# Optimization experiments

Measured on AMD Instinct MI355X. Metric: run time of the kernel, lower is better.

## Reference

```python
import jax, jax.numpy as jnp
import numpy as np

B, H, S, D = 2, 16, 2048, 128


def setup_inputs() -> dict:
    key = jax.random.key(0)
    kq, kk, kv = jax.random.split(key, 3)
    q = jax.random.normal(kq, (B, H, S, D), dtype=jnp.float32)
    k = jax.random.normal(kk, (B, H, S, D), dtype=jnp.float32)
    v = jax.random.normal(kv, (B, H, S, D), dtype=jnp.float32)
    scale = jnp.float32(1.0 / np.sqrt(D))
    return {"q": q, "k": k, "v": v, "scale": scale}


def reference(q, k, v, scale):
    # scores: [B, H, S, S]
    attn = jnp.einsum("bhqd,bhkd->bhqk", q, k) * scale
    attn = jnp.square(jax.nn.relu(attn))  # relu(x)^2 score function (no softmax)
    return jnp.einsum("bhqk,bhkd->bhqd", attn, v)
```

## Files before the change

### kernel.cpp

```cpp
#include <hip/hip_runtime.h>
#include <hip/hip_bf16.h>
#include <stdint.h>

#define S_LEN 2048
#define D_DIM 128
#define QT 128
#define KT 64
#define NT (S_LEN/KT)

typedef float  f32x4  __attribute__((ext_vector_type(4)));
typedef float  f32x16 __attribute__((ext_vector_type(16)));
typedef short  bf16x8 __attribute__((ext_vector_type(8)));
typedef unsigned int uintx4 __attribute__((ext_vector_type(4)));

__device__ __forceinline__ short f2bf(float f) {
    return __builtin_bit_cast(short, __float2bfloat16(f));
}

__device__ __forceinline__ unsigned int pk2(float lo, float hi) {
    unsigned int d;
    asm("v_cvt_pk_bf16_f32 %0, %1, %2" : "=v"(d) : "v"(lo), "v"(hi));
    return d;
}

__device__ __forceinline__ void gload_lds16(const short* g, char* l) {
    __builtin_amdgcn_global_load_lds(
        (const __attribute__((address_space(1))) void*)g,
        (__attribute__((address_space(3))) void*)l,
        16, 0, 0);
}

__global__ __launch_bounds__(256)
void convert_k_kernel(const float* __restrict__ kin, short* __restrict__ kbf) {
    const size_t i = ((size_t)blockIdx.x * 256 + threadIdx.x) * 8;
    f32x4 a = *(const f32x4*)(kin + i);
    f32x4 c = *(const f32x4*)(kin + i + 4);
    bf16x8 t;
    t[0]=f2bf(a[0]); t[1]=f2bf(a[1]); t[2]=f2bf(a[2]); t[3]=f2bf(a[3]);
    t[4]=f2bf(c[0]); t[5]=f2bf(c[1]); t[6]=f2bf(c[2]); t[7]=f2bf(c[3]);
    *(bf16x8*)(kbf + i) = t;
}

__global__ __launch_bounds__(256)
void transpose_v_kernel(const float* __restrict__ vin, short* __restrict__ vt) {
    __shared__ short T[16 * 130];
    const int tid = threadIdx.x;
    const int blk = blockIdx.x;
    const int bh  = blk >> 3;
    const int d0  = (blk & 7) * 16;
    const float* vb = vin + (size_t)bh * S_LEN * D_DIM;
    short* vtb = vt + (size_t)bh * (size_t)D_DIM * S_LEN;
    const int c4 = tid & 3;
    const int rr = tid >> 2;
    const int dl = tid >> 4;
    const int kc = tid & 15;

    for (int kc0 = 0; kc0 < S_LEN; kc0 += 128) {
        #pragma unroll
        for (int h = 0; h < 2; ++h) {
            const int krow = kc0 + h*64 + rr;
            f32x4 a = *(const f32x4*)(vb + (size_t)krow * D_DIM + d0 + c4*4);
            #pragma unroll
            for (int j = 0; j < 4; ++j)
                T[(c4*4 + j)*130 + h*64 + rr] = f2bf(a[j]);
        }
        __syncthreads();
        int w0 = *(const int*)&T[dl*130 + kc*8 + 0];
        int w1 = *(const int*)&T[dl*130 + kc*8 + 2];
        int w2 = *(const int*)&T[dl*130 + kc*8 + 4];
        int w3 = *(const int*)&T[dl*130 + kc*8 + 6];
        int4 val = make_int4(w0, w1, w2, w3);
        *(int4*)(vtb + (size_t)(d0 + dl) * S_LEN + kc0 + kc*8) = val;
        __syncthreads();
    }
}

__global__ __launch_bounds__(256, 2)
void relu2_attn_main(const float* __restrict__ q,
                     const short* __restrict__ kbf,
                     const short* __restrict__ vtbf,
                     const float* __restrict__ scale_p,
                     float* __restrict__ out) {
    __shared__ __align__(16) char lds[65536];

    const int tid  = threadIdx.x;
    const int wave = tid >> 6;
    const int lane = tid & 63;
    const int l31  = lane & 31;
    const int hi   = lane >> 5;

    const int bid = blockIdx.x;
    const int bh  = bid & 31;
    const int qt  = bid >> 5;
    const int q0  = qt * QT;

    const float* qb = q    + (size_t)bh * S_LEN * D_DIM;
    const short* kb = kbf  + (size_t)bh * S_LEN * D_DIM;
    const short* vt = vtbf + (size_t)bh * (size_t)D_DIM * S_LEN;
    float*       ob = out  + (size_t)bh * S_LEN * D_DIM;

    const float scale = scale_p[0];

    const int RB = hi*512 + l31*16;

    int kOff[4], vOff[4];
    #pragma unroll
    for (int p = 0; p < 4; ++p) {
        const int s = (p*4 + wave)*64 + lane;
        const int rK = ((s >> 9) << 5) | (s & 31);
        const int cK = (s >> 5) & 15;
        kOff[p] = rK*128 + cK*8;
        const int dV = (((s >> 8) & 3) << 5) | (s & 31);
        const int cV = (s >> 5) & 7;
        vOff[p] = dV*2048 + cV*8;
    }

    bf16x8 qa[8];
    {
        const int qrow = q0 + wave*32 + l31;
        const float* qp = qb + (size_t)qrow * D_DIM + hi*8;
        #pragma unroll
        for (int dk = 0; dk < 8; ++dk) {
            f32x4 a = *(const f32x4*)(qp + dk*16);
            f32x4 c = *(const f32x4*)(qp + dk*16 + 4);
            bf16x8 t;
            t[0]=f2bf(a[0]*scale); t[1]=f2bf(a[1]*scale);
            t[2]=f2bf(a[2]*scale); t[3]=f2bf(a[3]*scale);
            t[4]=f2bf(c[0]*scale); t[5]=f2bf(c[1]*scale);
            t[6]=f2bf(c[2]*scale); t[7]=f2bf(c[3]*scale);
            qa[dk] = t;
        }
    }

    f32x16 oacc[4];
    #pragma unroll
    for (int df = 0; df < 4; ++df) oacc[df] = {};

#define STAGE(T, B) do {                                                      \
    const int k0_ = (T) * KT;                                                 \
    _Pragma("unroll")                                                         \
    for (int p_ = 0; p_ < 4; ++p_) {                                          \
        const int ch_ = p_*4 + wave;                                          \
        gload_lds16(kb + k0_*128 + kOff[p_],                                  \
                    lds + (B)*16384 + ch_*1024);                              \
        gload_lds16(vt + k0_ + vOff[p_],                                      \
                    lds + 32768 + (B)*16384 + ch_*1024);                      \
    }                                                                         \
} while (0)

#define TILE_COMPUTE(BUF) do {                                                \
    f32x16 s0 = {}, s1 = {};                                                  \
    __builtin_amdgcn_s_setprio(1);                                            \
    _Pragma("unroll")                                                         \
    for (int dk = 0; dk < 8; ++dk) {                                          \
        bf16x8 a0 = *(const bf16x8*)(lds + (BUF)*16384 + RB + (dk<<10));      \
        bf16x8 a1 = *(const bf16x8*)(lds + (BUF)*16384 + RB + (dk<<10) + 8192); \
        s0 = __builtin_amdgcn_mfma_f32_32x32x16_bf16(a0, qa[dk], s0, 0, 0, 0);\
        s1 = __builtin_amdgcn_mfma_f32_32x32x16_bf16(a1, qa[dk], s1, 0, 0, 0);\
    }                                                                         \
    __builtin_amdgcn_s_setprio(0);                                            \
              \
    bf16x8 pa[4];                                                             \
    _Pragma("unroll")                                                         \
    for (int kf = 0; kf < 2; ++kf) {                                          \
        const f32x16 sv = kf ? s1 : s0;                                       \
        float pr[16];                                                         \
        _Pragma("unroll")                                                     \
        for (int r = 0; r < 16; ++r) {                                        \
            float m_ = fmaxf(sv[r], 0.f); pr[r] = m_ * m_;                    \
        }                                                                     \
        _Pragma("unroll")                                                     \
        for (int t2 = 0; t2 < 2; ++t2) {                                      \
            unsigned int X  = pk2(pr[8*t2+0], pr[8*t2+1]);                    \
            unsigned int Y  = pk2(pr[8*t2+4], pr[8*t2+5]);                    \
            unsigned int X2 = pk2(pr[8*t2+2], pr[8*t2+3]);                    \
            unsigned int Y2 = pk2(pr[8*t2+6], pr[8*t2+7]);                    \
            asm volatile("v_permlane32_swap_b32 %0, %1" : "+v"(X),  "+v"(Y)); \
            asm volatile("v_permlane32_swap_b32 %0, %1" : "+v"(X2), "+v"(Y2));\
            pa[kf*2 + t2] = __builtin_bit_cast(bf16x8, (uintx4){X, X2, Y, Y2});\
        }                                                                     \
    }                                                                         \
    __builtin_amdgcn_s_setprio(1);                                            \
    _Pragma("unroll")                                                         \
    for (int s_ = 0; s_ < 4; ++s_) {                                          \
        _Pragma("unroll")                                                     \
        for (int df = 0; df < 4; ++df) {                                      \
            bf16x8 vf = *(const bf16x8*)(lds + 32768 + (BUF)*16384 + RB       \
                                         + (df<<12) + (s_<<10));              \
            oacc[df] = __builtin_amdgcn_mfma_f32_32x32x16_bf16(pa[s_], vf, oacc[df], 0, 0, 0); \
        }                                                                     \
    }                                                                         \
    __builtin_amdgcn_s_setprio(0);                                            \
} while (0)

    STAGE(0, 0);

    #pragma unroll 1
    for (int p = 0; p < NT/2; ++p) {
        __syncthreads();
        STAGE(2*p + 1, 1);
        TILE_COMPUTE(0);
        __syncthreads();
        STAGE((2*p + 2) & (NT - 1), 0);
        TILE_COMPUTE(1);
    }

    #pragma unroll
    for (int df = 0; df < 4; ++df) {
        #pragma unroll
        for (int rg = 0; rg < 4; ++rg) {
            #pragma unroll
            for (int e = 0; e < 4; ++e) {
                const int row = q0 + wave*32 + rg*8 + hi*4 + e;
                ob[(size_t)row * D_DIM + df*32 + l31] = oacc[df][rg*4 + e];
            }
        }
    }
}

#define KS 136
#define VS 72
#define PS 72

__global__ __launch_bounds__(256, 2)
void relu2_attn_fallback(const float* __restrict__ q,
                         const float* __restrict__ k,
                         const float* __restrict__ v,
                         const float* __restrict__ scale_p,
                         float* __restrict__ out) {
    __shared__ short Klds[KT][KS];
    __shared__ short VTlds[D_DIM][VS];
    __shared__ short Plds[QT][PS];

    const int tid  = threadIdx.x;
    const int wave = tid >> 6;
    const int lane = tid & 63;
    const int l15  = lane & 15;
    const int lg   = lane >> 4;

    const int bid = blockIdx.x;
    const int bh  = bid & 31;
    const int qt  = bid >> 5;
    const int q0  = qt * QT;

    const float* qb = q + (size_t)bh * S_LEN * D_DIM;
    const float* kb = k + (size_t)bh * S_LEN * D_DIM;
    const float* vb = v + (size_t)bh * S_LEN * D_DIM;
    float*       ob = out + (size_t)bh * S_LEN * D_DIM;

    const float scale = scale_p[0];

    bf16x8 qa[2][4];
    {
        const int qrow = q0 + wave * 32;
        #pragma unroll
        for (int qf = 0; qf < 2; ++qf) {
            const float* qp = qb + (size_t)(qrow + qf*16 + l15) * D_DIM + lg * 8;
            #pragma unroll
            for (int dk = 0; dk < 4; ++dk) {
                f32x4 a = *(const f32x4*)(qp + dk*32);
                f32x4 c = *(const f32x4*)(qp + dk*32 + 4);
                bf16x8 t;
                t[0]=f2bf(a[0]*scale); t[1]=f2bf(a[1]*scale);
                t[2]=f2bf(a[2]*scale); t[3]=f2bf(a[3]*scale);
                t[4]=f2bf(c[0]*scale); t[5]=f2bf(c[1]*scale);
                t[6]=f2bf(c[2]*scale); t[7]=f2bf(c[3]*scale);
                qa[qf][dk] = t;
            }
        }
    }

    const int kr = tid >> 4;
    const int kc = tid & 15;
    const int vd = tid & 127;
    const int vh = (tid >> 7) * 32;

    f32x4 kreg[8];
    float vreg[32];

#define FLOAD_TILE(T) do {                                                    \
    const float* kp_ = kb + (size_t)((T) * KT) * D_DIM;                       \
    _Pragma("unroll")                                                         \
    for (int p = 0; p < 4; ++p) {                                             \
        const float* rp_ = kp_ + (size_t)(p*16 + kr) * D_DIM + kc*8;          \
        kreg[2*p]   = *(const f32x4*)rp_;                                     \
        kreg[2*p+1] = *(const f32x4*)(rp_ + 4);                               \
    }                                                                         \
    const float* vp_ = vb + (size_t)((T) * KT + vh) * D_DIM + vd;             \
    _Pragma("unroll")                                                         \
    for (int j = 0; j < 32; ++j) vreg[j] = vp_[(size_t)j * D_DIM];            \
} while (0)

#define FSTORE_TILE() do {                                                    \
    _Pragma("unroll")                                                         \
    for (int p = 0; p < 4; ++p) {                                             \
        f32x4 a_ = kreg[2*p], b_ = kreg[2*p+1];                               \
        bf16x8 w_;                                                            \
        w_[0]=f2bf(a_[0]); w_[1]=f2bf(a_[1]); w_[2]=f2bf(a_[2]); w_[3]=f2bf(a_[3]); \
        w_[4]=f2bf(b_[0]); w_[5]=f2bf(b_[1]); w_[6]=f2bf(b_[2]); w_[7]=f2bf(b_[3]); \
        *(bf16x8*)&Klds[p*16 + kr][kc*8] = w_;                                \
    }                                                                         \
    _Pragma("unroll")                                                         \
    for (int c = 0; c < 4; ++c) {                                             \
        bf16x8 w_;                                                            \
        w_[0]=f2bf(vreg[c*8+0]); w_[1]=f2bf(vreg[c*8+1]);                     \
        w_[2]=f2bf(vreg[c*8+2]); w_[3]=f2bf(vreg[c*8+3]);                     \
        w_[4]=f2bf(vreg[c*8+4]); w_[5]=f2bf(vreg[c*8+5]);                     \
        w_[6]=f2bf(vreg[c*8+6]); w_[7]=f2bf(vreg[c*8+7]);                     \
        *(bf16x8*)&VTlds[vd][vh + c*8] = w_;                                  \
    }                                                                         \
} while (0)

    f32x4 oacc[2][8];
    #pragma unroll
    for (int i = 0; i < 2; ++i)
        #pragma unroll
        for (int j = 0; j < 8; ++j)
            oacc[i][j] = f32x4{0.f, 0.f, 0.f, 0.f};

    FLOAD_TILE(0);

    for (int t = 0; t < NT; ++t) {
        FSTORE_TILE();
        __syncthreads();
        FLOAD_TILE((t + 1) & (NT - 1));

        f32x4 sacc[2][4];
        #pragma unroll
        for (int qf = 0; qf < 2; ++qf)
            #pragma unroll
            for (int kf = 0; kf < 4; ++kf)
                sacc[qf][kf] = f32x4{0.f, 0.f, 0.f, 0.f};

        #pragma unroll
        for (int dk = 0; dk < 4; ++dk) {
            #pragma unroll
            for (int kf = 0; kf < 4; ++kf) {
                bf16x8 bf = *(const bf16x8*)&Klds[kf*16 + l15][dk*32 + lg*8];
                #pragma unroll
                for (int qf = 0; qf < 2; ++qf)
                    sacc[qf][kf] = __builtin_amdgcn_mfma_f32_16x16x32_bf16(
                        qa[qf][dk], bf, sacc[qf][kf], 0, 0, 0);
            }
        }

        #pragma unroll
        for (int qf = 0; qf < 2; ++qf) {
            #pragma unroll
            for (int kf = 0; kf < 4; ++kf) {
                f32x4 sv = sacc[qf][kf];
                #pragma unroll
                for (int e = 0; e < 4; ++e) {
                    float r = fmaxf(sv[e], 0.f);
                    Plds[wave*32 + qf*16 + lg*4 + e][kf*16 + l15] = f2bf(r * r);
                }
            }
        }

        #pragma unroll
        for (int ks = 0; ks < 2; ++ks) {
            bf16x8 pa[2];
            #pragma unroll
            for (int qf = 0; qf < 2; ++qf)
                pa[qf] = *(const bf16x8*)&Plds[wave*32 + qf*16 + l15][ks*32 + lg*8];
            #pragma unroll
            for (int df = 0; df < 8; ++df) {
                bf16x8 vf = *(const bf16x8*)&VTlds[df*16 + l15][ks*32 + lg*8];
                #pragma unroll
                for (int qf = 0; qf < 2; ++qf)
                    oacc[qf][df] = __builtin_amdgcn_mfma_f32_16x16x32_bf16(
                        pa[qf], vf, oacc[qf][df], 0, 0, 0);
            }
        }
        __syncthreads();
    }

    #pragma unroll
    for (int qf = 0; qf < 2; ++qf) {
        #pragma unroll
        for (int df = 0; df < 8; ++df) {
            f32x4 o = oacc[qf][df];
            const int row = q0 + wave*32 + qf*16 + lg*4;
            float* op = ob + (size_t)row * D_DIM + df*16 + l15;
            op[0*D_DIM] = o[0];
            op[1*D_DIM] = o[1];
            op[2*D_DIM] = o[2];
            op[3*D_DIM] = o[3];
        }
    }
}

extern "C" void kernel_launch(void* const* d_in, const int* in_sizes, int n_in,
                              void* d_out, int out_size, void* d_ws, size_t ws_size,
                              hipStream_t stream) {
    const float* q = (const float*)d_in[0];
    const float* k = (const float*)d_in[1];
    const float* v = (const float*)d_in[2];
    const float* scale = (const float*)d_in[3];
    float* out = (float*)d_out;

    const size_t elems = (size_t)2 * 16 * S_LEN * D_DIM;
    const size_t need  = elems * 2 * 2;

    if (ws_size >= need) {
        short* kbf = (short*)d_ws;
        short* vtb = (short*)d_ws + elems;
        convert_k_kernel<<<dim3((int)(elems / (256 * 8))), dim3(256), 0, stream>>>(k, kbf);
        transpose_v_kernel<<<dim3(256), dim3(256), 0, stream>>>(v, vtb);
        relu2_attn_main<<<dim3(512), dim3(256), 0, stream>>>(q, kbf, vtb, scale, out);
    } else {
        relu2_attn_fallback<<<dim3(512), dim3(256), 0, stream>>>(q, k, v, scale, out);
    }
}
```

Measured before the change: 100.8 us.

## Split waves 2x2 over query and key halves to halve LDS fragment reads

Each wave now owns 64 query rows but only half of each 64-key tile, instead of 32 query rows over the full tile. Every K fragment read from LDS feeds two MFMAs (two query fragments), and every V fragment feeds two output accumulators. This cuts LDS read traffic per MFMA. The cost is twice the register footprint for Q fragments and output accumulators, plus an LDS reduction at the end where the two key-half waves sum their partial outputs. Register pressure at launch_bounds(256,2) may cause spills.

```diff
diff --git a/kernel.cpp b/kernel.cpp
--- a/kernel.cpp
+++ b/kernel.cpp
@@ -88,6 +88,8 @@
     const int lane = tid & 63;
     const int l31  = lane & 31;
     const int hi   = lane >> 5;
+    const int wq   = wave >> 1;
+    const int wk   = wave & 1;
 
     const int bid = blockIdx.x;
     const int bh  = bid & 31;
@@ -101,7 +103,9 @@
 
     const float scale = scale_p[0];
 
-    const int RB = hi*512 + l31*16;
+    const int RB   = hi*512 + l31*16;
+    const int KSEL = wk * 8192;
+    const int VSEL = wk * 2048;
 
     int kOff[4], vOff[4];
     #pragma unroll
@@ -115,9 +119,10 @@
         vOff[p] = dV*2048 + cV*8;
     }
 
-    bf16x8 qa[8];
-    {
-        const int qrow = q0 + wave*32 + l31;
+    bf16x8 qa[2][8];
+    #pragma unroll
+    for (int qf = 0; qf < 2; ++qf) {
+        const int qrow = q0 + wq*64 + qf*32 + l31;
         const float* qp = qb + (size_t)qrow * D_DIM + hi*8;
         #pragma unroll
         for (int dk = 0; dk < 8; ++dk) {
@@ -128,13 +133,15 @@
             t[2]=f2bf(a[2]*scale); t[3]=f2bf(a[3]*scale);
             t[4]=f2bf(c[0]*scale); t[5]=f2bf(c[1]*scale);
             t[6]=f2bf(c[2]*scale); t[7]=f2bf(c[3]*scale);
-            qa[dk] = t;
-        }
-    }
-
-    f32x16 oacc[4];
+            qa[qf][dk] = t;
+        }
+    }
+
+    f32x16 oacc[2][4];
     #pragma unroll
-    for (int df = 0; df < 4; ++df) oacc[df] = {};
+    for (int qf = 0; qf < 2; ++qf)
+        #pragma unroll
+        for (int df = 0; df < 4; ++df) oacc[qf][df] = {};
 
 #define STAGE(T, B) do {                                                      \
     const int k0_ = (T) * KT;                                                 \
@@ -148,46 +155,46 @@
     }                                                                         \
 } while (0)
 
+#define CONVERT_FRAG(SV, PA) do {                                             \
+    float pr[16];                                                             \
+    _Pragma("unroll")                                                         \
+    for (int r = 0; r < 16; ++r) {                                            \
+        float m_ = fmaxf((SV)[r], 0.f); pr[r] = m_ * m_;                      \
+    }                                                                         \
+    _Pragma("unroll")                                                         \
+    for (int t2 = 0; t2 < 2; ++t2) {                                          \
+        unsigned int X  = pk2(pr[8*t2+0], pr[8*t2+1]);                        \
+        unsigned int Y  = pk2(pr[8*t2+4], pr[8*t2+5]);                        \
+        unsigned int X2 = pk2(pr[8*t2+2], pr[8*t2+3]);                        \
+        unsigned int Y2 = pk2(pr[8*t2+6], pr[8*t2+7]);                        \
+        asm volatile("v_permlane32_swap_b32 %0, %1" : "+v"(X),  "+v"(Y));     \
+        asm volatile("v_permlane32_swap_b32 %0, %1" : "+v"(X2), "+v"(Y2));    \
+        (PA)[t2] = __builtin_bit_cast(bf16x8, (uintx4){X, X2, Y, Y2});        \
+    }                                                                         \
+} while (0)
+
 #define TILE_COMPUTE(BUF) do {                                                \
     f32x16 s0 = {}, s1 = {};                                                  \
     __builtin_amdgcn_s_setprio(1);                                            \
     _Pragma("unroll")                                                         \
     for (int dk = 0; dk < 8; ++dk) {                                          \
-        bf16x8 a0 = *(const bf16x8*)(lds + (BUF)*16384 + RB + (dk<<10));      \
-        bf16x8 a1 = *(const bf16x8*)(lds + (BUF)*16384 + RB + (dk<<10) + 8192); \
-        s0 = __builtin_amdgcn_mfma_f32_32x32x16_bf16(a0, qa[dk], s0, 0, 0, 0);\
-        s1 = __builtin_amdgcn_mfma_f32_32x32x16_bf16(a1, qa[dk], s1, 0, 0, 0);\
+        bf16x8 a = *(const bf16x8*)(lds + (BUF)*16384 + KSEL + RB + (dk<<10));\
+        s0 = __builtin_amdgcn_mfma_f32_32x32x16_bf16(a, qa[0][dk], s0, 0, 0, 0);\
+        s1 = __builtin_amdgcn_mfma_f32_32x32x16_bf16(a, qa[1][dk], s1, 0, 0, 0);\
     }                                                                         \
     __builtin_amdgcn_s_setprio(0);                                            \
-              \
-    bf16x8 pa[4];                                                             \
-    _Pragma("unroll")                                                         \
-    for (int kf = 0; kf < 2; ++kf) {                                          \
-        const f32x16 sv = kf ? s1 : s0;                                       \
-        float pr[16];                                                         \
-        _Pragma("unroll")                                                     \
-        for (int r = 0; r < 16; ++r) {                                        \
-            float m_ = fmaxf(sv[r], 0.f); pr[r] = m_ * m_;                    \
-        }                                                                     \
-        _Pragma("unroll")                                                     \
-        for (int t2 = 0; t2 < 2; ++t2) {                                      \
-            unsigned int X  = pk2(pr[8*t2+0], pr[8*t2+1]);                    \
-            unsigned int Y  = pk2(pr[8*t2+4], pr[8*t2+5]);                    \
-            unsigned int X2 = pk2(pr[8*t2+2], pr[8*t2+3]);                    \
-            unsigned int Y2 = pk2(pr[8*t2+6], pr[8*t2+7]);                    \
-            asm volatile("v_permlane32_swap_b32 %0, %1" : "+v"(X),  "+v"(Y)); \
-            asm volatile("v_permlane32_swap_b32 %0, %1" : "+v"(X2), "+v"(Y2));\
-            pa[kf*2 + t2] = __builtin_bit_cast(bf16x8, (uintx4){X, X2, Y, Y2});\
-        }                                                                     \
-    }                                                                         \
+    bf16x8 pa0[2], pa1[2];                                                    \
+    CONVERT_FRAG(s0, pa0);                                                    \
+    CONVERT_FRAG(s1, pa1);                                                    \
     __builtin_amdgcn_s_setprio(1);                                            \
     _Pragma("unroll")                                                         \
-    for (int s_ = 0; s_ < 4; ++s_) {                                          \
+    for (int t2 = 0; t2 < 2; ++t2) {                                          \
         _Pragma("unroll")                                                     \
         for (int df = 0; df < 4; ++df) {                                      \
             bf16x8 vf = *(const bf16x8*)(lds + 32768 + (BUF)*16384 + RB       \
-                                         + (df<<12) + (s_<<10));              \
-            oacc[df] = __builtin_amdgcn_mfma_f32_32x32x16_bf16(pa[s_], vf, oacc[df], 0, 0, 0); \
+                                         + (df<<12) + VSEL + (t2<<10));      \
+            oacc[0][df] = __builtin_amdgcn_mfma_f32_32x32x16_bf16(pa0[t2], vf, oacc[0][df], 0, 0, 0); \
+            oacc[1][df] = __builtin_amdgcn_mfma_f32_32x32x16_bf16(pa1[t2], vf, oacc[1][df], 0, 0, 0); \
         }                                                                     \
     }                                                                         \
     __builtin_amdgcn_s_setprio(0);                                            \
@@ -205,16 +212,36 @@
         TILE_COMPUTE(1);
     }
 
-    #pragma unroll
-    for (int df = 0; df < 4; ++df) {
-        #pragma unroll
-        for (int rg = 0; rg < 4; ++rg) {
-            #pragma unroll
-            for (int e = 0; e < 4; ++e) {
-                const int row = q0 + wave*32 + rg*8 + hi*4 + e;
-                ob[(size_t)row * D_DIM + df*32 + l31] = oacc[df][rg*4 + e];
-            }
-        }
+    __syncthreads();
+    float* Fl = (float*)lds;
+    if (wk == 1) {
+        #pragma unroll
+        for (int qf = 0; qf < 2; ++qf)
+            #pragma unroll
+            for (int df = 0; df < 4; ++df)
+                #pragma unroll
+                for (int rg = 0; rg < 4; ++rg)
+                    #pragma unroll
+                    for (int e = 0; e < 4; ++e)
+                        Fl[wq*8192 + (qf*32 + rg*8 + hi*4 + e)*128 + df*32 + l31]
+                            = oacc[qf][df][rg*4 + e];
+    }
+    __syncthreads();
+    if (wk == 0) {
+        #pragma unroll
+        for (int qf = 0; qf < 2; ++qf)
+            #pragma unroll
+            for (int df = 0; df < 4; ++df)
+                #pragma unroll
+                for (int rg = 0; rg < 4; ++rg)
+                    #pragma unroll
+                    for (int e = 0; e < 4; ++e) {
+                        const int qr = qf*32 + rg*8 + hi*4 + e;
+                        float v2 = Fl[wq*8192 + qr*128 + df*32 + l31];
+                        const int row = q0 + wq*64 + qr;
+                        ob[(size_t)row * D_DIM + df*32 + l31]
+                            = oacc[qf][df][rg*4 + e] + v2;
+                    }
     }
 }
 
```

Result: slower. 163.2 us (+61.8%).

## Halve KV tile to 32 keys and raise occupancy to four blocks per CU

Applied to the files above, without the earlier changes.

Reduces the K/V tile staged per iteration from 64 to 32 keys, which halves the LDS footprint to 32KB and drops one score accumulator. Launch bounds go from 2 to 4 blocks per CU. The staging offsets and LDS layout are reworked to match the smaller tile. The goal is more concurrent waves to hide memory latency, at the cost of twice as many loop iterations and barriers, and tighter register limits that may cause spills.

```diff
diff --git a/kernel.cpp b/kernel.cpp
--- a/kernel.cpp
+++ b/kernel.cpp
@@ -7,6 +7,8 @@
 #define QT 128
 #define KT 64
 #define NT (S_LEN/KT)
+#define TKT 32
+#define TNT (S_LEN/TKT)
 
 typedef float  f32x4  __attribute__((ext_vector_type(4)));
 typedef float  f32x16 __attribute__((ext_vector_type(16)));
@@ -75,13 +77,13 @@
     }
 }
 
-__global__ __launch_bounds__(256, 2)
+__global__ __launch_bounds__(256, 4)
 void relu2_attn_main(const float* __restrict__ q,
                      const short* __restrict__ kbf,
                      const short* __restrict__ vtbf,
                      const float* __restrict__ scale_p,
                      float* __restrict__ out) {
-    __shared__ __align__(16) char lds[65536];
+    __shared__ __align__(16) char lds[32768];
 
     const int tid  = threadIdx.x;
     const int wave = tid >> 6;
@@ -103,16 +105,13 @@
 
     const int RB = hi*512 + l31*16;
 
-    int kOff[4], vOff[4];
+    int kOff[2], vOff[2];
     #pragma unroll
-    for (int p = 0; p < 4; ++p) {
+    for (int p = 0; p < 2; ++p) {
         const int s = (p*4 + wave)*64 + lane;
-        const int rK = ((s >> 9) << 5) | (s & 31);
-        const int cK = (s >> 5) & 15;
-        kOff[p] = rK*128 + cK*8;
-        const int dV = (((s >> 8) & 3) << 5) | (s & 31);
-        const int cV = (s >> 5) & 7;
-        vOff[p] = dV*2048 + cV*8;
+        kOff[p] = (s & 31)*128 + (s >> 6)*16 + ((s >> 5) & 1)*8;
+        vOff[p] = ((s >> 7)*32 + (s & 31))*2048
+                + ((s >> 6) & 1)*16 + ((s >> 5) & 1)*8;
     }
 
     bf16x8 qa[8];
@@ -137,37 +136,33 @@
     for (int df = 0; df < 4; ++df) oacc[df] = {};
 
 #define STAGE(T, B) do {                                                      \
-    const int k0_ = (T) * KT;                                                 \
-    _Pragma("unroll")                                                         \
-    for (int p_ = 0; p_ < 4; ++p_) {                                          \
+    const int k0_ = (T) * TKT;                                                \
+    _Pragma("unroll")                                                         \
+    for (int p_ = 0; p_ < 2; ++p_) {                                          \
         const int ch_ = p_*4 + wave;                                          \
-        gload_lds16(kb + k0_*128 + kOff[p_],                                  \
-                    lds + (B)*16384 + ch_*1024);                              \
+        gload_lds16(kb + (size_t)k0_*128 + kOff[p_],                          \
+                    lds + (B)*8192 + ch_*1024);                               \
         gload_lds16(vt + k0_ + vOff[p_],                                      \
-                    lds + 32768 + (B)*16384 + ch_*1024);                      \
+                    lds + 16384 + (B)*8192 + ch_*1024);                       \
     }                                                                         \
 } while (0)
 
 #define TILE_COMPUTE(BUF) do {                                                \
-    f32x16 s0 = {}, s1 = {};                                                  \
+    f32x16 s0 = {};                                                           \
     __builtin_amdgcn_s_setprio(1);                                            \
     _Pragma("unroll")                                                         \
     for (int dk = 0; dk < 8; ++dk) {                                          \
-        bf16x8 a0 = *(const bf16x8*)(lds + (BUF)*16384 + RB + (dk<<10));      \
-        bf16x8 a1 = *(const bf16x8*)(lds + (BUF)*16384 + RB + (dk<<10) + 8192); \
-        s0 = __builtin_amdgcn_mfma_f32_32x32x16_bf16(a0, qa[dk], s0, 0, 0, 0);\
-        s1 = __builtin_amdgcn_mfma_f32_32x32x16_bf16(a1, qa[dk], s1, 0, 0, 0);\
+        bf16x8 a = *(const bf16x8*)(lds + (BUF)*8192 + RB + (dk<<10));        \
+        s0 = __builtin_amdgcn_mfma_f32_32x32x16_bf16(a, qa[dk], s0, 0, 0, 0); \
     }                                                                         \
     __builtin_amdgcn_s_setprio(0);                                            \
               \
-    bf16x8 pa[4];                                                             \
-    _Pragma("unroll")                                                         \
-    for (int kf = 0; kf < 2; ++kf) {                                          \
-        const f32x16 sv = kf ? s1 : s0;                                       \
+    bf16x8 pa[2];                                                             \
+    {                                                                         \
         float pr[16];                                                         \
         _Pragma("unroll")                                                     \
         for (int r = 0; r < 16; ++r) {                                        \
-            float m_ = fmaxf(sv[r], 0.f); pr[r] = m_ * m_;                    \
+            float m_ = fmaxf(s0[r], 0.f); pr[r] = m_ * m_;                    \
         }                                                                     \
         _Pragma("unroll")                                                     \
         for (int t2 = 0; t2 < 2; ++t2) {                                      \
@@ -177,17 +172,18 @@
             unsigned int Y2 = pk2(pr[8*t2+6], pr[8*t2+7]);                    \
             asm volatile("v_permlane32_swap_b32 %0, %1" : "+v"(X),  "+v"(Y)); \
             asm volatile("v_permlane32_swap_b32 %0, %1" : "+v"(X2), "+v"(Y2));\
-            pa[kf*2 + t2] = __builtin_bit_cast(bf16x8, (uintx4){X, X2, Y, Y2});\
+            pa[t2] = __builtin_bit_cast(bf16x8, (uintx4){X, X2, Y, Y2});      \
         }                                                                     \
     }                                                                         \
     __builtin_amdgcn_s_setprio(1);                                            \
     _Pragma("unroll")                                                         \
-    for (int s_ = 0; s_ < 4; ++s_) {                                          \
+    for (int s_ = 0; s_ < 2; ++s_) {                                          \
         _Pragma("unroll")                                                     \
         for (int df = 0; df < 4; ++df) {                                      \
-            bf16x8 vf = *(const bf16x8*)(lds + 32768 + (BUF)*16384 + RB       \
-                                         + (df<<12) + (s_<<10));              \
-            oacc[df] = __builtin_amdgcn_mfma_f32_32x32x16_bf16(pa[s_], vf, oacc[df], 0, 0, 0); \
+            bf16x8 vf = *(const bf16x8*)(lds + 16384 + (BUF)*8192 + RB        \
+                                         + (df<<11) + (s_<<10));              \
+            oacc[df] = __builtin_amdgcn_mfma_f32_32x32x16_bf16(               \
+                           pa[s_], vf, oacc[df], 0, 0, 0);                    \
         }                                                                     \
     }                                                                         \
     __builtin_amdgcn_s_setprio(0);                                            \
@@ -196,12 +192,12 @@
     STAGE(0, 0);
 
     #pragma unroll 1
-    for (int p = 0; p < NT/2; ++p) {
+    for (int p = 0; p < TNT/2; ++p) {
         __syncthreads();
         STAGE(2*p + 1, 1);
         TILE_COMPUTE(0);
         __syncthreads();
-        STAGE((2*p + 2) & (NT - 1), 0);
+        STAGE((2*p + 2) & (TNT - 1), 0);
         TILE_COMPUTE(1);
     }
 
```

Measured after the change: 114.5 us. 13.5% more time.

## Use two waves per block, each computing two 32-row Q fragments to reuse K/V

Applied to the files above, without the earlier changes.

The main kernel now runs 128 threads (2 waves) instead of 4, and each wave handles 64 query rows as two 32-row fragments. Each K and V LDS fragment read then feeds two MFMAs, halving LDS read traffic per MFMA. The LDS staging layout changes to match, and each thread issues 8 async loads per stage instead of 4. The cost is about double the accumulator and Q registers, and fewer waves per block to hide latency, with the launch bound set to 1 block per SIMD-level hint.

```diff
diff --git a/kernel.cpp b/kernel.cpp
--- a/kernel.cpp
+++ b/kernel.cpp
@@ -21,6 +21,11 @@
     unsigned int d;
     asm("v_cvt_pk_bf16_f32 %0, %1, %2" : "=v"(d) : "v"(lo), "v"(hi));
     return d;
+}
+
+__device__ __forceinline__ float r2(float x) {
+    float m = fmaxf(x, 0.f);
+    return m * m;
 }
 
 __device__ __forceinline__ void gload_lds16(const short* g, char* l) {
@@ -75,7 +80,7 @@
     }
 }
 
-__global__ __launch_bounds__(256, 2)
+__global__ __launch_bounds__(128, 1)
 void relu2_attn_main(const float* __restrict__ q,
                      const short* __restrict__ kbf,
                      const short* __restrict__ vtbf,
@@ -103,21 +108,18 @@
 
     const int RB = hi*512 + l31*16;
 
-    int kOff[4], vOff[4];
-    #pragma unroll
-    for (int p = 0; p < 4; ++p) {
-        const int s = (p*4 + wave)*64 + lane;
-        const int rK = ((s >> 9) << 5) | (s & 31);
-        const int cK = (s >> 5) & 15;
-        kOff[p] = rK*128 + cK*8;
-        const int dV = (((s >> 8) & 3) << 5) | (s & 31);
-        const int cV = (s >> 5) & 7;
-        vOff[p] = dV*2048 + cV*8;
-    }
-
-    bf16x8 qa[8];
-    {
-        const int qrow = q0 + wave*32 + l31;
+    int kOff[8], vOff[8];
+    #pragma unroll
+    for (int p = 0; p < 8; ++p) {
+        const int f = p*2 + wave;
+        kOff[p] = ((f & 1)*32 + l31)*128 + (f >> 1)*16 + hi*8;
+        vOff[p] = ((f >> 2)*32 + l31)*2048 + (f & 3)*16 + hi*8;
+    }
+
+    bf16x8 qa[2][8];
+    #pragma unroll
+    for (int qf = 0; qf < 2; ++qf) {
+        const int qrow = q0 + wave*64 + qf*32 + l31;
         const float* qp = qb + (size_t)qrow * D_DIM + hi*8;
         #pragma unroll
         for (int dk = 0; dk < 8; ++dk) {
@@ -128,66 +130,75 @@
             t[2]=f2bf(a[2]*scale); t[3]=f2bf(a[3]*scale);
             t[4]=f2bf(c[0]*scale); t[5]=f2bf(c[1]*scale);
             t[6]=f2bf(c[2]*scale); t[7]=f2bf(c[3]*scale);
-            qa[dk] = t;
-        }
-    }
-
-    f32x16 oacc[4];
-    #pragma unroll
-    for (int df = 0; df < 4; ++df) oacc[df] = {};
-
-#define STAGE(T, B) do {                                                      \
+            qa[qf][dk] = t;
+        }
+    }
+
+    f32x16 oacc[2][4];
+    #pragma unroll
+    for (int qf = 0; qf < 2; ++qf)
+        #pragma unroll
+        for (int df = 0; df < 4; ++df) oacc[qf][df] = {};
+
+#define STAGE(T, CB) do {                                                     \
     const int k0_ = (T) * KT;                                                 \
     _Pragma("unroll")                                                         \
-    for (int p_ = 0; p_ < 4; ++p_) {                                          \
-        const int ch_ = p_*4 + wave;                                          \
-        gload_lds16(kb + k0_*128 + kOff[p_],                                  \
-                    lds + (B)*16384 + ch_*1024);                              \
+    for (int p_ = 0; p_ < 8; ++p_) {                                          \
+        const int ch_ = p_*2 + wave;                                          \
+        gload_lds16(kb + (size_t)k0_*128 + kOff[p_],                          \
+                    lds + (CB) + ch_*1024);                                   \
         gload_lds16(vt + k0_ + vOff[p_],                                      \
-                    lds + 32768 + (B)*16384 + ch_*1024);                      \
+                    lds + (CB) + 16384 + ch_*1024);                           \
     }                                                                         \
 } while (0)
 
-#define TILE_COMPUTE(BUF) do {                                                \
-    f32x16 s0 = {}, s1 = {};                                                  \
+#define CONV(SV, P0, P1) do {                                                 \
+    unsigned int X, Y, X2, Y2;                                                \
+    X  = pk2(r2((SV)[0]), r2((SV)[1]));                                       \
+    Y  = pk2(r2((SV)[4]), r2((SV)[5]));                                       \
+    X2 = pk2(r2((SV)[2]), r2((SV)[3]));                                       \
+    Y2 = pk2(r2((SV)[6]), r2((SV)[7]));                                       \
+    asm volatile("v_permlane32_swap_b32 %0, %1" : "+v"(X),  "+v"(Y));         \
+    asm volatile("v_permlane32_swap_b32 %0, %1" : "+v"(X2), "+v"(Y2));        \
+    (P0) = __builtin_bit_cast(bf16x8, (uintx4){X, X2, Y, Y2});                \
+    X  = pk2(r2((SV)[8]),  r2((SV)[9]));                                      \
+    Y  = pk2(r2((SV)[12]), r2((SV)[13]));                                     \
+    X2 = pk2(r2((SV)[10]), r2((SV)[11]));                                     \
+    Y2 = pk2(r2((SV)[14]), r2((SV)[15]));                                     \
+    asm volatile("v_permlane32_swap_b32 %0, %1" : "+v"(X),  "+v"(Y));         \
+    asm volatile("v_permlane32_swap_b32 %0, %1" : "+v"(X2), "+v"(Y2));        \
+    (P1) = __builtin_bit_cast(bf16x8, (uintx4){X, X2, Y, Y2});                \
+} while (0)
+
+#define TILE_COMPUTE(CB) do {                                                 \
+    f32x16 s00 = {}, s01 = {}, s10 = {}, s11 = {};                            \
     __builtin_amdgcn_s_setprio(1);                                            \
     _Pragma("unroll")                                                         \
     for (int dk = 0; dk < 8; ++dk) {                                          \
-        bf16x8 a0 = *(const bf16x8*)(lds + (BUF)*16384 + RB + (dk<<10));      \
-        bf16x8 a1 = *(const bf16x8*)(lds + (BUF)*16384 + RB + (dk<<10) + 8192); \
-        s0 = __builtin_amdgcn_mfma_f32_32x32x16_bf16(a0, qa[dk], s0, 0, 0, 0);\
-        s1 = __builtin_amdgcn_mfma_f32_32x32x16_bf16(a1, qa[dk], s1, 0, 0, 0);\
+        bf16x8 a0 = *(const bf16x8*)(lds + (CB) + ((dk*2+0)<<10) + RB);       \
+        bf16x8 a1 = *(const bf16x8*)(lds + (CB) + ((dk*2+1)<<10) + RB);       \
+        s00 = __builtin_amdgcn_mfma_f32_32x32x16_bf16(a0, qa[0][dk], s00, 0, 0, 0); \
+        s10 = __builtin_amdgcn_mfma_f32_32x32x16_bf16(a0, qa[1][dk], s10, 0, 0, 0); \
+        s01 = __builtin_amdgcn_mfma_f32_32x32x16_bf16(a1, qa[0][dk], s01, 0, 0, 0); \
+        s11 = __builtin_amdgcn_mfma_f32_32x32x16_bf16(a1, qa[1][dk], s11, 0, 0, 0); \
     }                                                                         \
     __builtin_amdgcn_s_setprio(0);                                            \
-              \
-    bf16x8 pa[4];                                                             \
-    _Pragma("unroll")                                                         \
-    for (int kf = 0; kf < 2; ++kf) {                                          \
-        const f32x16 sv = kf ? s1 : s0;                                       \
-        float pr[16];                                                         \
-        _Pragma("unroll")                                                     \
-        for (int r = 0; r < 16; ++r) {                                        \
-            float m_ = fmaxf(sv[r], 0.f); pr[r] = m_ * m_;                    \
-        }                                                                     \
-        _Pragma("unroll")                                                     \
-        for (int t2 = 0; t2 < 2; ++t2) {                                      \
-            unsigned int X  = pk2(pr[8*t2+0], pr[8*t2+1]);                    \
-            unsigned int Y  = pk2(pr[8*t2+4], pr[8*t2+5]);                    \
-            unsigned int X2 = pk2(pr[8*t2+2], pr[8*t2+3]);                    \
-            unsigned int Y2 = pk2(pr[8*t2+6], pr[8*t2+7]);                    \
-            asm volatile("v_permlane32_swap_b32 %0, %1" : "+v"(X),  "+v"(Y)); \
-            asm volatile("v_permlane32_swap_b32 %0, %1" : "+v"(X2), "+v"(Y2));\
-            pa[kf*2 + t2] = __builtin_bit_cast(bf16x8, (uintx4){X, X2, Y, Y2});\
-        }                                                                     \
-    }                                                                         \
+    bf16x8 pa[2][4];                                                          \
+    CONV(s00, pa[0][0], pa[0][1]);                                            \
+    CONV(s01, pa[0][2], pa[0][3]);                                            \
+    CONV(s10, pa[1][0], pa[1][1]);                                            \
+    CONV(s11, pa[1][2], pa[1][3]);                                            \
     __builtin_amdgcn_s_setprio(1);                                            \
     _Pragma("unroll")                                                         \
-    for (int s_ = 0; s_ < 4; ++s_) {                                          \
+    for (int ks = 0; ks < 4; ++ks) {                                          \
         _Pragma("unroll")                                                     \
         for (int df = 0; df < 4; ++df) {                                      \
-            bf16x8 vf = *(const bf16x8*)(lds + 32768 + (BUF)*16384 + RB       \
-                                         + (df<<12) + (s_<<10));              \
-            oacc[df] = __builtin_amdgcn_mfma_f32_32x32x16_bf16(pa[s_], vf, oacc[df], 0, 0, 0); \
+            bf16x8 vf = *(const bf16x8*)(lds + (CB) + 16384                   \
+                                         + ((df*4+ks)<<10) + RB);             \
+            oacc[0][df] = __builtin_amdgcn_mfma_f32_32x32x16_bf16(            \
+                              pa[0][ks], vf, oacc[0][df], 0, 0, 0);           \
+            oacc[1][df] = __builtin_amdgcn_mfma_f32_32x32x16_bf16(            \
+                              pa[1][ks], vf, oacc[1][df], 0, 0, 0);           \
         }                                                                     \
     }                                                                         \
     __builtin_amdgcn_s_setprio(0);                                            \
@@ -198,21 +209,24 @@
     #pragma unroll 1
     for (int p = 0; p < NT/2; ++p) {
         __syncthreads();
-        STAGE(2*p + 1, 1);
+        STAGE(2*p + 1, 32768);
         TILE_COMPUTE(0);
         __syncthreads();
         STAGE((2*p + 2) & (NT - 1), 0);
-        TILE_COMPUTE(1);
-    }
-
-    #pragma unroll
-    for (int df = 0; df < 4; ++df) {
-        #pragma unroll
-        for (int rg = 0; rg < 4; ++rg) {
-            #pragma unroll
-            for (int e = 0; e < 4; ++e) {
-                const int row = q0 + wave*32 + rg*8 + hi*4 + e;
-                ob[(size_t)row * D_DIM + df*32 + l31] = oacc[df][rg*4 + e];
+        TILE_COMPUTE(32768);
+    }
+
+    #pragma unroll
+    for (int qf = 0; qf < 2; ++qf) {
+        #pragma unroll
+        for (int df = 0; df < 4; ++df) {
+            #pragma unroll
+            for (int rg = 0; rg < 4; ++rg) {
+                #pragma unroll
+                for (int e = 0; e < 4; ++e) {
+                    const int row = q0 + wave*64 + qf*32 + rg*8 + hi*4 + e;
+                    ob[(size_t)row * D_DIM + df*32 + l31] = oacc[qf][df][rg*4 + e];
+                }
             }
         }
     }
@@ -407,7 +421,7 @@
         short* vtb = (short*)d_ws + elems;
         convert_k_kernel<<<dim3((int)(elems / (256 * 8))), dim3(256), 0, stream>>>(k, kbf);
         transpose_v_kernel<<<dim3(256), dim3(256), 0, stream>>>(v, vtb);
-        relu2_attn_main<<<dim3(512), dim3(256), 0, stream>>>(q, kbf, vtb, scale, out);
+        relu2_attn_main<<<dim3(512), dim3(128), 0, stream>>>(q, kbf, vtb, scale, out);
     } else {
         relu2_attn_fallback<<<dim3(512), dim3(256), 0, stream>>>(q, k, v, scale, out);
     }
```

Result: slower. 108.9 us (+8.0%).
